# Optimization experiments

Measured on AMD Instinct MI355X. Metric: run time of the kernel, lower is better.

## Reference

```python
import jax, jax.numpy as jnp
import numpy as np

B, T, C, H, E, MIN_E = 4, 2048, 1024, 128, 16, 2
IS_CAUSAL = False


def setup_inputs() -> dict:
    key = jax.random.key(0)
    ks = jax.random.split(key, 6)
    lim_qkv = float(np.sqrt(6.0 / (C + H)))
    inp = {
        "hidden_states": jax.random.normal(ks[0], (B, T, C), jnp.float32),
        "sim_matrix": jax.random.normal(ks[1], (C, E), jnp.float32),
        "gates": jnp.zeros((E,), jnp.float32),
        "q_proj": jax.random.uniform(ks[2], (E, C, H), jnp.float32, -lim_qkv, lim_qkv),
        "k_proj": jax.random.uniform(ks[3], (E, C, H), jnp.float32, -lim_qkv, lim_qkv),
        "v_proj": jax.random.uniform(ks[4], (E, C, H), jnp.float32, -lim_qkv, lim_qkv),
        "o_proj": jax.random.uniform(ks[5], (E, H, C), jnp.float32, -lim_qkv, lim_qkv),
    }
    return inp


def _forward(hidden_states, sim_matrix, gates, q_proj, k_proj, v_proj, o_proj):
    b, t, c = hidden_states.shape
    n = b * t
    x = hidden_states.reshape(n, c)

    # ---- gating (faithful to _gating_logic) ----
    xn = x / jnp.maximum(jnp.linalg.norm(x, axis=-1, keepdims=True), 1e-12)
    sn = sim_matrix / jnp.maximum(jnp.linalg.norm(sim_matrix, axis=0, keepdims=True), 1e-12)
    logits = xn @ sn - jax.nn.sigmoid(gates)          # [n, E]
    gated = jax.nn.relu(logits)
    # STE: forward = (gated > 0), backward = identity
    hard = (gated > 0).astype(gated.dtype)
    mask = gated + jax.lax.stop_gradient(hard - gated)
    inactive = (jnp.sum(hard, axis=1) == 0)
    # fallback: top-MIN_E logits for tokens with no active expert
    _, fb_idx = jax.lax.top_k(logits, MIN_E)
    fb = jnp.zeros((n, logits.shape[1]), gated.dtype).at[
        jnp.arange(n)[:, None], fb_idx].set(1.0)
    put = jax.lax.stop_gradient(inactive[:, None].astype(gated.dtype) * fb)
    mask = mask * (1.0 - put) + put                   # index_put semantics
    masked = jnp.where(mask > 0, gated, -jnp.inf)
    w = jax.nn.softmax(masked, axis=-1)               # routing weights [n, E]

    # ---- MoE dispatch/combine (dense-equivalent: w is exactly 0 where mask==0) ----
    def moe_proj(p):  # p: [E, C, H] -> [n, H]
        y = jnp.einsum('nc,ech->neh', x, p)
        return jnp.einsum('ne,neh->nh', w, y)

    q = moe_proj(q_proj).reshape(b, t, -1)
    k = moe_proj(k_proj).reshape(b, t, -1)
    v = moe_proj(v_proj).reshape(b, t, -1)

    # single-head SDPA, default scale 1/sqrt(head_dim)
    h = q.shape[-1]
    scores = jnp.einsum('bth,bsh->bts', q, k) / jnp.sqrt(jnp.asarray(h, q.dtype))
    if IS_CAUSAL and t > 1:
        causal = jnp.tril(jnp.ones((t, t), bool))
        scores = jnp.where(causal[None], scores, -jnp.inf)
    attn = jax.nn.softmax(scores, axis=-1)
    o = jnp.einsum('bts,bsh->bth', attn, v).reshape(n, h)

    # output MoE combine
    z = jnp.einsum('ne,nh->enh', w, o)                # [E, n, H]
    out = jnp.einsum('enh,ehc->nc', z, o_proj)
    return out.reshape(b, t, c)


def reference(hidden_states, sim_matrix, gates, q_proj, k_proj, v_proj, o_proj):
    return _forward(hidden_states, sim_matrix, gates, q_proj, k_proj, v_proj, o_proj)
```

## Files before the change

### kernel.cpp

```cpp
#include <hip/hip_runtime.h>
#include <hip/hip_bf16.h>
#include <math.h>

#define NBATCH 4
#define NT     2048
#define NC     1024
#define NH     128
#define NE     16
#define NTOK   (NBATCH * NT)
#define CAP    18432
#define NT2_MAX 152

typedef __bf16 bf16x8 __attribute__((ext_vector_type(8)));
typedef __bf16 bf16x4 __attribute__((ext_vector_type(4)));
typedef float  f32x4  __attribute__((ext_vector_type(4)));

__device__ __forceinline__ __bf16 f2bf(float f) { return (__bf16)f; }

#define BARRIER() __builtin_amdgcn_s_barrier()
#define SFENCE()  __builtin_amdgcn_sched_barrier(0)
#define VMWAIT(n) asm volatile("s_waitcnt vmcnt(" #n ")" ::: "memory")
#define LGKMWAIT0() asm volatile("s_waitcnt lgkmcnt(0)" ::: "memory")

__device__ __forceinline__ void gl_lds16(const void* g, void* l) {
  __builtin_amdgcn_global_load_lds((const __attribute__((address_space(1))) void*)g,
                                   (__attribute__((address_space(3))) void*)l, 16, 0, 0);
}

__device__ __forceinline__ const __bf16* swz_src(const __bf16* row0, size_t stride,
                                                 int tid, int i) {
  int lin = (tid + 256 * i) * 16;
  int r = lin >> 7, cb = lin & 127;
  return row0 + (size_t)r * stride + ((cb ^ ((r & 7) << 4)) >> 1);
}

__global__ void k_transpose_all(const float* __restrict__ qp, const float* __restrict__ kp,
                                const float* __restrict__ vp, const float* __restrict__ op,
                                __bf16* __restrict__ pqt, __bf16* __restrict__ pkt,
                                __bf16* __restrict__ pvt, __bf16* __restrict__ pot,
                                const float* __restrict__ sim, const float* __restrict__ gates,
                                double* __restrict__ snorm, double* __restrict__ sig) {
  __shared__ float tile[32][33];
  __shared__ double red[16][17];
  int z = blockIdx.y;
  int tid = threadIdx.x;
  if (z == 64) {
    if (blockIdx.x != 0) return;
    int e = tid & 15, chunk = tid >> 4;
    double a = 0.0;
#pragma unroll 4
    for (int j = 0; j < 64; j++) {
      double v = (double)sim[(chunk * 64 + j) * NE + e];
      a += v * v;
    }
    red[chunk][e] = a;
    __syncthreads();
    if (tid < 16) {
      double s = 0.0;
      for (int k = 0; k < 16; k++) s += red[k][tid];
      snorm[tid] = fmax(sqrt(s), 1e-12);
      sig[tid] = 1.0 / (1.0 + exp(-(double)gates[tid]));
    }
    return;
  }
  const float* in;
  __bf16* out;
  int R, Cd, g, r0, c0;
  if (z < 48) {
    int which = z >> 4; g = z & 15; R = 1024; Cd = 128;
    in = which == 0 ? qp : (which == 1 ? kp : vp);
    out = which == 0 ? pqt : (which == 1 ? pkt : pvt);
    r0 = (blockIdx.x >> 2) * 32; c0 = (blockIdx.x & 3) * 32;
  } else {
    g = z - 48; R = 128; Cd = 1024;
    in = op; out = pot;
    r0 = (blockIdx.x & 3) * 32; c0 = (blockIdx.x >> 2) * 32;
  }
  int tx = tid & 31, ty0 = tid >> 5;
  const float* src = in + (size_t)g * R * Cd;
  __bf16* dst = out + (size_t)g * R * Cd;
#pragma unroll
  for (int ty = ty0; ty < 32; ty += 8)
    tile[ty][tx] = src[(size_t)(r0 + ty) * Cd + (c0 + tx)];
  __syncthreads();
#pragma unroll
  for (int ty = ty0; ty < 32; ty += 8)
    dst[(size_t)(c0 + ty) * R + (r0 + tx)] = f2bf(tile[tx][ty]);
}

__global__ __launch_bounds__(256, 2) void k_gating3(const float* __restrict__ x,
                                                    const float* __restrict__ sim,
                                                    const double* __restrict__ snorm,
                                                    const double* __restrict__ sig,
                                                    float* __restrict__ w_all,
                                                    int* __restrict__ counts,
                                                    __bf16* __restrict__ xbf) {
  __shared__ union {
    struct {
      float xs_[16][66];
      float ss_[16][66];
    } s;
    double red[8][32][2][17];
  } u;
  __shared__ float w_lds[16][16];
  __shared__ int cnt_lds[16];
  int tid = threadIdx.x;
  if (tid < 16) cnt_lds[tid] = 0;
  int cg = tid & 31, tkg = tid >> 5;
  int tok0 = blockIdx.x * 16;

  double acc[2][17];
#pragma unroll
  for (int t = 0; t < 2; t++)
#pragma unroll
    for (int i = 0; i < 17; i++) acc[t][i] = 0.0;

  int xr0 = tid >> 4, xc4 = (tid & 15) * 4;
  int sr = tid >> 2, se4 = (tid & 3) * 4;

  float4 xa, sv;
  auto ldchunk = [&](int c0) {
    xa = *(const float4*)(x + (size_t)(tok0 + xr0) * NC + c0 + xc4);
    sv = *(const float4*)(sim + (size_t)(c0 + sr) * NE + se4);
  };
  auto stchunk = [&]() {
    *(float4*)&u.s.xs_[xr0][xc4] = xa;
    u.s.ss_[se4 + 0][sr] = sv.x;
    u.s.ss_[se4 + 1][sr] = sv.y;
    u.s.ss_[se4 + 2][sr] = sv.z;
    u.s.ss_[se4 + 3][sr] = sv.w;
  };
  auto stxbf = [&](int c0) {
    bf16x4 a;
    a[0]=f2bf(xa.x); a[1]=f2bf(xa.y); a[2]=f2bf(xa.z); a[3]=f2bf(xa.w);
    *(bf16x4*)(xbf + (size_t)(tok0 + xr0) * NC + c0 + xc4) = a;
  };

  ldchunk(0);
  for (int ch = 0; ch < 16; ch++) {
    stchunk();
    stxbf(ch * 64);
    __syncthreads();
    if (ch < 15) ldchunk((ch + 1) * 64);
    double xd[2][2];
#pragma unroll
    for (int t = 0; t < 2; t++) {
      float2 xv = *(const float2*)&u.s.xs_[tkg * 2 + t][cg * 2];
      xd[t][0] = (double)xv.x;
      xd[t][1] = (double)xv.y;
      acc[t][16] += xd[t][0] * xd[t][0] + xd[t][1] * xd[t][1];
    }
#pragma unroll
    for (int e = 0; e < 16; e++) {
      float2 sv2 = *(const float2*)&u.s.ss_[e][cg * 2];
      double s0 = (double)sv2.x, s1 = (double)sv2.y;
#pragma unroll
      for (int t = 0; t < 2; t++)
        acc[t][e] += xd[t][0] * s0 + xd[t][1] * s1;
    }
    __syncthreads();
  }

#pragma unroll
  for (int t = 0; t < 2; t++)
#pragma unroll
    for (int i = 0; i < 17; i++)
      u.red[tkg][cg][t][i] = acc[t][i];
  __syncthreads();

  if (tid < 16) {
    double dots[17];
    for (int i = 0; i < 17; i++) {
      double s = 0.0;
      for (int c = 0; c < 32; c++) s += u.red[tid >> 1][c][tid & 1][i];
      dots[i] = s;
    }
    double xn = fmax(sqrt(dots[16]), 1e-12);
    double logits[NE];
    unsigned act = 0;
    int cnt = 0;
    for (int ee = 0; ee < NE; ee++) {
      logits[ee] = dots[ee] / (xn * snorm[ee]) - sig[ee];
      if (logits[ee] > 0.0) { act |= 1u << ee; cnt++; }
    }
    if (cnt == 0) {
      int i1 = 0; double b1 = logits[0];
      for (int ee = 1; ee < NE; ee++) if (logits[ee] > b1) { b1 = logits[ee]; i1 = ee; }
      int i2 = -1; double b2 = -1e300;
      for (int ee = 0; ee < NE; ee++) if (ee != i1 && logits[ee] > b2) { b2 = logits[ee]; i2 = ee; }
      act = (1u << i1) | (1u << i2);
    }
    double m = -1e300;
    for (int ee = 0; ee < NE; ee++) if ((act >> ee) & 1) m = fmax(m, fmax(logits[ee], 0.0));
    double s = 0.0, wvv[NE];
    for (int ee = 0; ee < NE; ee++) {
      if ((act >> ee) & 1) { wvv[ee] = exp(fmax(logits[ee], 0.0) - m); s += wvv[ee]; }
      else wvv[ee] = 0.0;
    }
    for (int ee = 0; ee < NE; ee++) {
      if ((act >> ee) & 1) {
        w_lds[tid][ee] = (float)(wvv[ee] / s);
        atomicAdd(&cnt_lds[ee], 1);
      } else w_lds[tid][ee] = 0.0f;
    }
  }
  __syncthreads();
  w_all[(size_t)(tok0 + (tid >> 4)) * NE + (tid & 15)] = w_lds[tid >> 4][tid & 15];
  if (tid < 16 && cnt_lds[tid] > 0) atomicAdd(&counts[tid], cnt_lds[tid]);
}

__global__ void k_transpose_bf(const __bf16* __restrict__ in, __bf16* __restrict__ out,
                               int R, int Cd) {
  __shared__ __bf16 tile[32][34];
  int g = blockIdx.z;
  int r0 = blockIdx.x * 32, c0 = blockIdx.y * 32;
  int tx = threadIdx.x & 31, ty0 = threadIdx.x >> 5;
  const __bf16* src = in + (size_t)g * R * Cd;
  __bf16* dst = out + (size_t)g * R * Cd;
#pragma unroll
  for (int ty = ty0; ty < 32; ty += 8)
    tile[ty][tx] = src[(size_t)(r0 + ty) * Cd + (c0 + tx)];
  __syncthreads();
#pragma unroll
  for (int ty = ty0; ty < 32; ty += 8)
    dst[(size_t)(c0 + ty) * R + (r0 + tx)] = tile[tx][ty];
}

__global__ void k_scan(const int* __restrict__ counts, int* __restrict__ offsets,
                       int2* __restrict__ tile_desc, int* __restrict__ n_tiles) {
  if (threadIdx.x == 0 && blockIdx.x == 0) {
    int off = 0, nt = 0;
    for (int e = 0; e < NE; e++) {
      offsets[e] = off;
      int c = counts[e];
      int tiles = (c + 127) >> 7;
      for (int t = 0; t < tiles; t++) {
        int s0 = off + t * 128;
        if (s0 < CAP && nt < NT2_MAX) { tile_desc[nt].x = e; tile_desc[nt].y = s0; nt++; }
      }
      off += c;
    }
    offsets[NE] = off;
    *n_tiles = nt;
  }
}

__global__ void k_assign(const float* __restrict__ w_all, const int* __restrict__ offsets,
                         int* __restrict__ cursors, int* __restrict__ slot_token,
                         float* __restrict__ slot_w, int* __restrict__ tok_slots,
                         int* __restrict__ tok_cnt) {
  int n = blockIdx.x * 256 + threadIdx.x;
  if (n >= NTOK) return;
  int j = 0;
  for (int e = 0; e < NE; e++) {
    float w = w_all[(size_t)n * NE + e];
    if (w > 0.0f) {
      int p = atomicAdd(&cursors[e], 1);
      int s = offsets[e] + p;
      slot_token[s] = n;
      slot_w[s] = w;
      tok_slots[n * 16 + j] = s;
      j++;
    }
  }
  tok_cnt[n] = j;
}

__device__ __forceinline__ void mfma_block(const __bf16* As, const __bf16* Bs,
                                           int lane, int wrow, f32x4 acc[8]) {
  const char* Ab = (const char*)As;
  const char* Bb = (const char*)Bs;
  int arow = wrow + (lane & 15);
  int rb = lane & 15;
#pragma unroll
  for (int ks = 0; ks < 2; ks++) {
    int kb = ks * 64 + (lane >> 4) * 16;
    bf16x8 af = *(const bf16x8*)(Ab + arow * 128 + (kb ^ ((arow & 7) << 4)));
#pragma unroll
    for (int nt = 0; nt < 8; nt++) {
      int brow = nt * 16 + rb;
      bf16x8 bv = *(const bf16x8*)(Bb + brow * 128 + (kb ^ ((brow & 7) << 4)));
      acc[nt] = __builtin_amdgcn_mfma_f32_16x16x32_bf16(af, bv, acc[nt], 0, 0, 0);
    }
  }
}

__device__ __forceinline__ void mfma_block128(const __bf16* As, const __bf16* Bs,
                                              int lane, int wrow2, f32x4 acc[2][8]) {
  const char* Ab = (const char*)As;
  const char* Bb = (const char*)Bs;
  int rb = lane & 15;
#pragma unroll
  for (int ks = 0; ks < 2; ks++) {
    int kb = ks * 64 + (lane >> 4) * 16;
    int ar = wrow2 + rb;
    int sw = kb ^ ((ar & 7) << 4);
    bf16x8 af0 = *(const bf16x8*)(Ab + ar * 128 + sw);
    bf16x8 af1 = *(const bf16x8*)(Ab + (ar + 16) * 128 + sw);
#pragma unroll
    for (int nt = 0; nt < 8; nt++) {
      int brow = nt * 16 + rb;
      bf16x8 bv = *(const bf16x8*)(Bb + brow * 128 + (kb ^ ((brow & 7) << 4)));
      acc[0][nt] = __builtin_amdgcn_mfma_f32_16x16x32_bf16(af0, bv, acc[0][nt], 0, 0, 0);
      acc[1][nt] = __builtin_amdgcn_mfma_f32_16x16x32_bf16(af1, bv, acc[1][nt], 0, 0, 0);
    }
  }
}

__device__ __forceinline__ void mfma_regA(bf16x8 af0, bf16x8 af1, const __bf16* Bs,
                                          int lane, f32x4 acc[8]) {
  const char* Bb = (const char*)Bs;
  int rb = lane & 15;
#pragma unroll
  for (int ks = 0; ks < 2; ks++) {
    int kb = ks * 64 + (lane >> 4) * 16;
    bf16x8 af = ks ? af1 : af0;
#pragma unroll
    for (int nt = 0; nt < 8; nt++) {
      int brow = nt * 16 + rb;
      bf16x8 bv = *(const bf16x8*)(Bb + brow * 128 + (kb ^ ((brow & 7) << 4)));
      acc[nt] = __builtin_amdgcn_mfma_f32_16x16x32_bf16(af, bv, acc[nt], 0, 0, 0);
    }
  }
}

__global__ __launch_bounds__(256) void k_moe_qkv2(
    const __bf16* __restrict__ xbf, const int* __restrict__ slot_token,
    const __bf16* __restrict__ pq, const __bf16* __restrict__ pk, const __bf16* __restrict__ pv,
    const int* __restrict__ offsets, const int2* __restrict__ tile_desc,
    const int* __restrict__ n_tiles,
    __bf16* __restrict__ yq, __bf16* __restrict__ yk, __bf16* __restrict__ yv) {
  int id = blockIdx.x;
  int w = (id & 7) * (3 * NT2_MAX / 8) + (id >> 3);
  int ti = w / 3, p = w % 3;
  if (ti >= *n_tiles) return;
  int2 td = tile_desc[ti];
  int e = td.x, s0 = td.y;
  int seg_end = offsets[e + 1]; if (seg_end > CAP) seg_end = CAP;
  const __bf16* Bt;
  __bf16* Yd;
  if (p == 0)      { Bt = pq; Yd = yq; }
  else if (p == 1) { Bt = pk; Yd = yk; }
  else             { Bt = pv; Yd = yv; }
  Bt += (size_t)e * NH * NC;

  __shared__ __bf16 As[2][128 * 64];
  __shared__ __bf16 Bs[2][128 * 64];
  int tid = threadIdx.x, lane = tid & 63, wid = tid >> 6, wrow2 = wid * 32;
  const __bf16* asrc[4];
  const __bf16* bsrc[4];
#pragma unroll
  for (int i = 0; i < 4; i++) {
    int lin = (tid + 256 * i) * 16;
    int r = lin >> 7, cb = lin & 127;
    int tok = slot_token[s0 + r] & (NTOK - 1);
    asrc[i] = xbf + (size_t)tok * NC + ((cb ^ ((r & 7) << 4)) >> 1);
  }
#pragma unroll
  for (int i = 0; i < 4; i++) bsrc[i] = swz_src(Bt, NC, tid, i);
  auto stage = [&](int buf, int k0) {
#pragma unroll
    for (int i = 0; i < 4; i++)
      gl_lds16(asrc[i] + k0, (char*)As[buf] + tid * 16 + i * 4096);
#pragma unroll
    for (int i = 0; i < 4; i++)
      gl_lds16(bsrc[i] + k0, (char*)Bs[buf] + tid * 16 + i * 4096);
  };

  f32x4 acc[2][8];
#pragma unroll
  for (int rf = 0; rf < 2; rf++)
#pragma unroll
    for (int i = 0; i < 8; i++) { f32x4 z = {0.f, 0.f, 0.f, 0.f}; acc[rf][i] = z; }

  stage(0, 0);
  stage(1, 64);
  VMWAIT(8); BARRIER(); SFENCE();
  int cur = 0;
  for (int t = 0; t <= 13; t++) {
    __builtin_amdgcn_s_setprio(1);
    mfma_block128(As[cur], Bs[cur], lane, wrow2, acc);
    __builtin_amdgcn_s_setprio(0);
    SFENCE();
    BARRIER();
    stage(cur, (t + 2) * 64);
    VMWAIT(8); BARRIER(); SFENCE();
    cur ^= 1;
  }
  __builtin_amdgcn_s_setprio(1);
  mfma_block128(As[cur], Bs[cur], lane, wrow2, acc);
  __builtin_amdgcn_s_setprio(0);
  SFENCE();
  VMWAIT(0); BARRIER(); SFENCE();
  __builtin_amdgcn_s_setprio(1);
  mfma_block128(As[cur ^ 1], Bs[cur ^ 1], lane, wrow2, acc);
  __builtin_amdgcn_s_setprio(0);

  int col = lane & 15, quad = lane >> 4;
#pragma unroll
  for (int rf = 0; rf < 2; rf++)
#pragma unroll
    for (int r = 0; r < 4; r++) {
      int s = s0 + wrow2 + rf * 16 + quad * 4 + r;
      if (s < seg_end) {
#pragma unroll
        for (int nt = 0; nt < 8; nt++)
          Yd[(size_t)s * NH + nt * 16 + col] = f2bf(acc[rf][nt][r]);
      }
    }
}

__global__ __launch_bounds__(256) void k_combine_qkv(
    const __bf16* __restrict__ yq, const __bf16* __restrict__ yk, const __bf16* __restrict__ yv,
    const int* __restrict__ tok_slots, const int* __restrict__ tok_cnt,
    const float* __restrict__ slot_w,
    __bf16* __restrict__ qb, __bf16* __restrict__ kb, __bf16* __restrict__ vb) {
  int token = blockIdx.x * 2 + (threadIdx.x >> 7);
  int h = threadIdx.x & 127;
  const __bf16* Y;
  __bf16* D;
  float sc = 1.0f;
  if (blockIdx.y == 0)      { Y = yq; D = qb; sc = 0.12751744458115337f; }
  else if (blockIdx.y == 1) { Y = yk; D = kb; }
  else                      { Y = yv; D = vb; }
  int cnt = tok_cnt[token];
  float acc = 0.f;
  for (int j = 0; j < cnt; j++) {
    int s = tok_slots[token * 16 + j];
    if (s < CAP) acc += slot_w[s] * (float)Y[(size_t)s * NH + h];
  }
  D[(size_t)token * NH + h] = f2bf(acc * sc);
}

__global__ __launch_bounds__(256) void k_flash(const __bf16* __restrict__ q,
                                               const __bf16* __restrict__ k,
                                               const __bf16* __restrict__ vt,
                                               float* __restrict__ opart,
                                               float2* __restrict__ ml) {
  int id = blockIdx.x;
  int w = (id & 7) * 64 + (id >> 3);
  int b = w >> 7;
  int rem = w & 127;
  int spl = rem >> 5;
  int t0 = (rem & 31) * 64;
  const __bf16* qb = q + (size_t)b * NT * NH;
  const __bf16* kb = k + (size_t)b * NT * NH;
  const __bf16* vtb = vt + (size_t)b * NH * NT;

  __shared__ __bf16 Ks[2][128 * 64];
  __shared__ __bf16 Vs[2][128 * 64];
  __shared__ __bf16 Ps[2][64 * 64];
  int tid = threadIdx.x, lane = tid & 63, wid = tid >> 6, wrow = wid * 16;
  int colq = lane & 15, quad = lane >> 4;

  bf16x8 qf[4];
  {
    const __bf16* qr = qb + (size_t)(t0 + wrow + colq) * NH + quad * 8;
#pragma unroll
    for (int kk = 0; kk < 4; kk++) qf[kk] = *(const bf16x8*)(qr + kk * 32);
  }
  asm volatile("" :: "v"(qf[0]), "v"(qf[1]), "v"(qf[2]), "v"(qf[3]));
  SFENCE();

  auto stage_K = [&](int s0) {
#pragma unroll
    for (int c = 0; c < 2; c++)
#pragma unroll
      for (int i = 0; i < 4; i++)
        gl_lds16(swz_src(kb + (size_t)s0 * NH + c * 64, NH, tid, i),
                 (char*)Ks[c] + wid * 1024 + i * 4096);
  };
  auto stage_V = [&](int s0) {
#pragma unroll
    for (int c = 0; c < 2; c++)
#pragma unroll
      for (int i = 0; i < 4; i++)
        gl_lds16(swz_src(vtb + s0 + c * 64, NT, tid, i),
                 (char*)Vs[c] + wid * 1024 + i * 4096);
  };

  f32x4 oacc[8];
#pragma unroll
  for (int i = 0; i < 8; i++) { f32x4 z = {0.f, 0.f, 0.f, 0.f}; oacc[i] = z; }
  float mr[4], lr[4];
#pragma unroll
  for (int r = 0; r < 4; r++) { mr[r] = -1e30f; lr[r] = 0.f; }

  const int sbase = spl * 512;
  stage_K(sbase);
  stage_V(sbase);
  VMWAIT(8); BARRIER(); SFENCE();

  for (int t = 0; t < 4; t++) {
    f32x4 sacc[8];
#pragma unroll
    for (int i = 0; i < 8; i++) { f32x4 z = {0.f, 0.f, 0.f, 0.f}; sacc[i] = z; }
    __builtin_amdgcn_s_setprio(1);
    mfma_regA(qf[0], qf[1], Ks[0], lane, sacc);
    mfma_regA(qf[2], qf[3], Ks[1], lane, sacc);
    __builtin_amdgcn_s_setprio(0);
    SFENCE();
    BARRIER();
    if (t < 3) stage_K(sbase + (t + 1) * 128);

    float tm[4];
#pragma unroll
    for (int r = 0; r < 4; r++) {
      float v = sacc[0][r];
#pragma unroll
      for (int nt = 1; nt < 8; nt++) v = fmaxf(v, sacc[nt][r]);
      tm[r] = v;
    }
#pragma unroll
    for (int off = 1; off < 16; off <<= 1)
#pragma unroll
      for (int r = 0; r < 4; r++) tm[r] = fmaxf(tm[r], __shfl_xor(tm[r], off));
    float alpha[4], rs[4];
#pragma unroll
    for (int r = 0; r < 4; r++) {
      float mn = fmaxf(mr[r], tm[r]);
      alpha[r] = exp2f(mr[r] - mn);
      mr[r] = mn;
      rs[r] = 0.f;
    }
#pragma unroll
    for (int nt = 0; nt < 8; nt++) {
      char* pc = (char*)Ps[nt >> 2];
      int colb = ((nt & 3) * 16 + colq) * 2;
#pragma unroll
      for (int r = 0; r < 4; r++) {
        int row = wrow + quad * 4 + r;
        float p = exp2f(sacc[nt][r] - mr[r]);
        rs[r] += p;
        *(__bf16*)(pc + row * 128 + (colb ^ ((row & 7) << 4))) = f2bf(p);
      }
    }
#pragma unroll
    for (int off = 1; off < 16; off <<= 1)
#pragma unroll
      for (int r = 0; r < 4; r++) rs[r] += __shfl_xor(rs[r], off);
#pragma unroll
    for (int r = 0; r < 4; r++) lr[r] = alpha[r] * lr[r] + rs[r];
#pragma unroll
    for (int nt = 0; nt < 8; nt++)
#pragma unroll
      for (int r = 0; r < 4; r++) oacc[nt][r] *= alpha[r];

    LGKMWAIT0();
    if (t < 3) { VMWAIT(8); } else { VMWAIT(0); }
    BARRIER(); SFENCE();

    __builtin_amdgcn_s_setprio(1);
    mfma_block(Ps[0], Vs[0], lane, wrow, oacc);
    mfma_block(Ps[1], Vs[1], lane, wrow, oacc);
    __builtin_amdgcn_s_setprio(0);
    SFENCE();
    BARRIER();
    if (t < 3) {
      stage_V(sbase + (t + 1) * 128);
      VMWAIT(8); BARRIER(); SFENCE();
    }
  }

  size_t base = (size_t)(b * 4 + spl) * NT + t0;
#pragma unroll
  for (int r = 0; r < 4; r++) {
    size_t row = base + wrow + quad * 4 + r;
#pragma unroll
    for (int nt = 0; nt < 8; nt++)
      opart[row * NH + nt * 16 + colq] = oacc[nt][r];
  }
  if (colq == 0) {
#pragma unroll
    for (int r = 0; r < 4; r++) {
      float2 v; v.x = mr[r]; v.y = lr[r];
      ml[base + wrow + quad * 4 + r] = v;
    }
  }
}

__global__ __launch_bounds__(256) void k_gather_o(const float* __restrict__ opart,
                                                  const float2* __restrict__ ml,
                                                  const int* __restrict__ slot_token,
                                                  const int* __restrict__ offsets,
                                                  __bf16* __restrict__ og) {
  int slot = blockIdx.x * 2 + (threadIdx.x >> 7);
  int h = threadIdx.x & 127;
  int total = offsets[NE]; if (total > CAP) total = CAP;
  if (slot >= total) return;
  int n = slot_token[slot];
  int b = n >> 11, trow = n & 2047;
  size_t rb = (size_t)b * 4 * NT + trow;
  float2 m0 = ml[rb], m1 = ml[rb + NT], m2 = ml[rb + 2 * NT], m3 = ml[rb + 3 * NT];
  float M = fmaxf(fmaxf(m0.x, m1.x), fmaxf(m2.x, m3.x));
  float e0 = exp2f(m0.x - M), e1 = exp2f(m1.x - M), e2 = exp2f(m2.x - M), e3 = exp2f(m3.x - M);
  float den = m0.y * e0 + m1.y * e1 + m2.y * e2 + m3.y * e3;
  float num = opart[rb * NH + h] * e0 + opart[(rb + NT) * NH + h] * e1 +
              opart[(rb + 2 * NT) * NH + h] * e2 + opart[(rb + 3 * NT) * NH + h] * e3;
  og[(size_t)slot * NH + h] = f2bf(num / den);
}

__global__ __launch_bounds__(256) void k_out2(
    const __bf16* __restrict__ og, const __bf16* __restrict__ pot,
    const int* __restrict__ offsets, const int2* __restrict__ tile_desc,
    const int* __restrict__ n_tiles, __bf16* __restrict__ zy) {
  int id = blockIdx.x;
  int w = (id & 7) * NT2_MAX + (id >> 3);
  int ti = w >> 3, p = w & 7;
  if (ti >= *n_tiles) return;
  int2 td = tile_desc[ti];
  int e = td.x, s0 = td.y;
  int seg_end = offsets[e + 1]; if (seg_end > CAP) seg_end = CAP;
  int nc0 = p * 128;
  const __bf16* Bt = pot + (size_t)e * NC * NH;

  __shared__ __bf16 As[2][128 * 64];
  __shared__ __bf16 Bs[2][128 * 64];
  int tid = threadIdx.x, lane = tid & 63, wid = tid >> 6, wrow2 = wid * 32;
  const __bf16* asrc[4];
  const __bf16* bsrc[4];
#pragma unroll
  for (int i = 0; i < 4; i++) asrc[i] = swz_src(og + (size_t)s0 * NH, NH, tid, i);
#pragma unroll
  for (int i = 0; i < 4; i++) bsrc[i] = swz_src(Bt + (size_t)nc0 * NH, NH, tid, i);
  auto stage = [&](int buf, int k0) {
#pragma unroll
    for (int i = 0; i < 4; i++)
      gl_lds16(asrc[i] + k0, (char*)As[buf] + tid * 16 + i * 4096);
#pragma unroll
    for (int i = 0; i < 4; i++)
      gl_lds16(bsrc[i] + k0, (char*)Bs[buf] + tid * 16 + i * 4096);
  };
  f32x4 acc[2][8];
#pragma unroll
  for (int rf = 0; rf < 2; rf++)
#pragma unroll
    for (int i = 0; i < 8; i++) { f32x4 z = {0.f, 0.f, 0.f, 0.f}; acc[rf][i] = z; }

  stage(0, 0);
  stage(1, 64);
  VMWAIT(8); BARRIER(); SFENCE();
  __builtin_amdgcn_s_setprio(1);
  mfma_block128(As[0], Bs[0], lane, wrow2, acc);
  __builtin_amdgcn_s_setprio(0);
  SFENCE();
  VMWAIT(0); BARRIER(); SFENCE();
  __builtin_amdgcn_s_setprio(1);
  mfma_block128(As[1], Bs[1], lane, wrow2, acc);
  __builtin_amdgcn_s_setprio(0);

  int col = lane & 15, quad = lane >> 4;
#pragma unroll
  for (int rf = 0; rf < 2; rf++)
#pragma unroll
    for (int r = 0; r < 4; r++) {
      int s = s0 + wrow2 + rf * 16 + quad * 4 + r;
      if (s < seg_end) {
#pragma unroll
        for (int nt = 0; nt < 8; nt++)
          zy[(size_t)s * NC + nc0 + nt * 16 + col] = f2bf(acc[rf][nt][r]);
      }
    }
}

__global__ __launch_bounds__(256) void k_combine_out(
    const __bf16* __restrict__ zy, const int* __restrict__ tok_slots,
    const int* __restrict__ tok_cnt, const float* __restrict__ slot_w,
    float* __restrict__ out) {
  int token = blockIdx.x;
  int c = threadIdx.x * 4;
  int cnt = tok_cnt[token];
  float a0 = 0.f, a1 = 0.f, a2 = 0.f, a3 = 0.f;
  for (int j = 0; j < cnt; j++) {
    int s = tok_slots[token * 16 + j];
    if (s < CAP) {
      float w = slot_w[s];
      bf16x4 z = *(const bf16x4*)&zy[(size_t)s * NC + c];
      a0 += w * (float)z[0];
      a1 += w * (float)z[1];
      a2 += w * (float)z[2];
      a3 += w * (float)z[3];
    }
  }
  float4 o = {a0, a1, a2, a3};
  *(float4*)&out[(size_t)token * NC + c] = o;
}

extern "C" void kernel_launch(void* const* d_in, const int* in_sizes, int n_in,
                              void* d_out, int out_size, void* d_ws, size_t ws_size,
                              hipStream_t stream) {
  const float* hs    = (const float*)d_in[0];
  const float* sim   = (const float*)d_in[1];
  const float* gates = (const float*)d_in[2];
  const float* qp    = (const float*)d_in[3];
  const float* kp    = (const float*)d_in[4];
  const float* vp    = (const float*)d_in[5];
  const float* op    = (const float*)d_in[6];
  float* out = (float*)d_out;
  char* ws = (char*)d_ws;

  const size_t M = 1048576;
  __bf16* PQT = (__bf16*)(ws + 0 * M);
  __bf16* PKT = (__bf16*)(ws + 4 * M);
  __bf16* PVT = (__bf16*)(ws + 8 * M);
  __bf16* POT = (__bf16*)(ws + 12 * M);
  __bf16* Qb  = (__bf16*)(ws + 16 * M);
  __bf16* Kb  = (__bf16*)(ws + 18 * M);
  __bf16* Vb  = (__bf16*)(ws + 20 * M);
  __bf16* VT  = (__bf16*)(ws + 22 * M);
  float*  WALL = (float*)(ws + 28 * M);
  int*    STOK = (int*)(ws + 28 * M + 524288);
  float*  SW   = (float*)(ws + 28 * M + 1048576);
  int*    TSL  = (int*)(ws + 28 * M + 1572864);
  int*    TCN  = (int*)(ws + 28 * M + 2097152);
  double* SNORM = (double*)(ws + 28 * M + 2129920);
  double* SIG   = SNORM + 16;
  int* CNT = (int*)(ws + 28 * M + 2130432);
  int* OFF = CNT + 16;
  int* CUR = CNT + 40;
  int* NTL = CNT + 60;
  int2* DESC = (int2*)(ws + 28 * M + 2131456);
  __bf16* XBF = (__bf16*)(ws + 32 * M);
  __bf16* YQ = (__bf16*)(ws + 72 * M);
  __bf16* YK = (__bf16*)(ws + 77 * M);
  __bf16* YV = (__bf16*)(ws + 82 * M);
  float*  OP2 = (float*)(ws + 32 * M);
  float2* MLB = (float2*)(ws + 50 * M);
  __bf16* OG = (__bf16*)(ws + 52 * M);
  __bf16* ZY = (__bf16*)(ws + 60 * M);

  hipMemsetAsync(CNT, 0, 512, stream);

  k_transpose_all<<<dim3(128, 65), 256, 0, stream>>>(qp, kp, vp, op, PQT, PKT, PVT, POT,
                                                     sim, gates, SNORM, SIG);
  k_gating3<<<NTOK / 16, 256, 0, stream>>>(hs, sim, SNORM, SIG, WALL, CNT, XBF);
  k_scan<<<1, 64, 0, stream>>>(CNT, OFF, DESC, NTL);
  k_assign<<<NTOK / 256, 256, 0, stream>>>(WALL, OFF, CUR, STOK, SW, TSL, TCN);
  k_moe_qkv2<<<3 * NT2_MAX, 256, 0, stream>>>(XBF, STOK, PQT, PKT, PVT, OFF, DESC, NTL, YQ, YK, YV);
  k_combine_qkv<<<dim3(NTOK / 2, 3), 256, 0, stream>>>(YQ, YK, YV, TSL, TCN, SW, Qb, Kb, Vb);
  k_transpose_bf<<<dim3(64, 4, 4), 256, 0, stream>>>(Vb, VT, 2048, 128);
  k_flash<<<512, 256, 0, stream>>>(Qb, Kb, VT, OP2, MLB);
  k_gather_o<<<CAP / 2, 256, 0, stream>>>(OP2, MLB, STOK, OFF, OG);
  k_out2<<<8 * NT2_MAX, 256, 0, stream>>>(OG, POT, OFF, DESC, NTL, ZY);
  k_combine_out<<<NTOK, 256, 0, stream>>>(ZY, TSL, TCN, SW, out);
}
```

Measured before the change: 286.2 us.

## Fuse V transpose into QKV combine, widen out-proj tiles, drop memset

The QKV combine kernel now handles 32 tokens per block with 16-wide vectorized bf16 loads. For V it transposes through LDS and writes V^T directly, which removes the separate transpose kernel and the Vb round trip. The output projection kernel computes two 128-column chunks per block, reusing the staged A tile and halving the grid. The counter memset is folded into the first kernel, saving one launch but adding ordering reliance on that kernel.

```diff
diff --git a/kernel.cpp b/kernel.cpp
--- a/kernel.cpp
+++ b/kernel.cpp
@@ -39,13 +39,15 @@
                                 __bf16* __restrict__ pqt, __bf16* __restrict__ pkt,
                                 __bf16* __restrict__ pvt, __bf16* __restrict__ pot,
                                 const float* __restrict__ sim, const float* __restrict__ gates,
-                                double* __restrict__ snorm, double* __restrict__ sig) {
+                                double* __restrict__ snorm, double* __restrict__ sig,
+                                int* __restrict__ ctrl) {
   __shared__ float tile[32][33];
   __shared__ double red[16][17];
   int z = blockIdx.y;
   int tid = threadIdx.x;
   if (z == 64) {
     if (blockIdx.x != 0) return;
+    if (tid < 128) ctrl[tid] = 0;
     int e = tid & 15, chunk = tid >> 4;
     double a = 0.0;
 #pragma unroll 4
@@ -209,23 +211,6 @@
   if (tid < 16 && cnt_lds[tid] > 0) atomicAdd(&counts[tid], cnt_lds[tid]);
 }
 
-__global__ void k_transpose_bf(const __bf16* __restrict__ in, __bf16* __restrict__ out,
-                               int R, int Cd) {
-  __shared__ __bf16 tile[32][34];
-  int g = blockIdx.z;
-  int r0 = blockIdx.x * 32, c0 = blockIdx.y * 32;
-  int tx = threadIdx.x & 31, ty0 = threadIdx.x >> 5;
-  const __bf16* src = in + (size_t)g * R * Cd;
-  __bf16* dst = out + (size_t)g * R * Cd;
-#pragma unroll
-  for (int ty = ty0; ty < 32; ty += 8)
-    tile[ty][tx] = src[(size_t)(r0 + ty) * Cd + (c0 + tx)];
-  __syncthreads();
-#pragma unroll
-  for (int ty = ty0; ty < 32; ty += 8)
-    dst[(size_t)(c0 + ty) * R + (r0 + tx)] = tile[tx][ty];
-}
-
 __global__ void k_scan(const int* __restrict__ counts, int* __restrict__ offsets,
                        int2* __restrict__ tile_desc, int* __restrict__ n_tiles) {
   if (threadIdx.x == 0 && blockIdx.x == 0) {
@@ -414,22 +399,49 @@
     const __bf16* __restrict__ yq, const __bf16* __restrict__ yk, const __bf16* __restrict__ yv,
     const int* __restrict__ tok_slots, const int* __restrict__ tok_cnt,
     const float* __restrict__ slot_w,
-    __bf16* __restrict__ qb, __bf16* __restrict__ kb, __bf16* __restrict__ vb) {
-  int token = blockIdx.x * 2 + (threadIdx.x >> 7);
-  int h = threadIdx.x & 127;
-  const __bf16* Y;
-  __bf16* D;
-  float sc = 1.0f;
-  if (blockIdx.y == 0)      { Y = yq; D = qb; sc = 0.12751744458115337f; }
-  else if (blockIdx.y == 1) { Y = yk; D = kb; }
-  else                      { Y = yv; D = vb; }
-  int cnt = tok_cnt[token];
-  float acc = 0.f;
+    __bf16* __restrict__ qb, __bf16* __restrict__ kb, __bf16* __restrict__ vt) {
+  __shared__ __bf16 vtile[128][34];
+  int tid = threadIdx.x;
+  int tok0 = blockIdx.x * 32;
+  int tt = tok0 + (tid >> 3);
+  int h0 = (tid & 7) * 16;
+  const __bf16* Y = blockIdx.y == 0 ? yq : (blockIdx.y == 1 ? yk : yv);
+  int cnt = tok_cnt[tt];
+  float acc[16];
+#pragma unroll
+  for (int i = 0; i < 16; i++) acc[i] = 0.f;
   for (int j = 0; j < cnt; j++) {
-    int s = tok_slots[token * 16 + j];
-    if (s < CAP) acc += slot_w[s] * (float)Y[(size_t)s * NH + h];
-  }
-  D[(size_t)token * NH + h] = f2bf(acc * sc);
+    int s = tok_slots[tt * 16 + j];
+    if (s < CAP) {
+      float w = slot_w[s];
+      bf16x8 v0 = *(const bf16x8*)(Y + (size_t)s * NH + h0);
+      bf16x8 v1 = *(const bf16x8*)(Y + (size_t)s * NH + h0 + 8);
+#pragma unroll
+      for (int i = 0; i < 8; i++) { acc[i] += w * (float)v0[i]; acc[8 + i] += w * (float)v1[i]; }
+    }
+  }
+  if (blockIdx.y == 2) {
+#pragma unroll
+    for (int i = 0; i < 16; i++) vtile[h0 + i][tid >> 3] = f2bf(acc[i]);
+    __syncthreads();
+    int h = tid >> 1, tp = (tid & 1) * 16;
+    int b = tok0 >> 11, trow = tok0 & 2047;
+    __bf16* dst = vt + ((size_t)b * NH + h) * NT + trow + tp;
+    bf16x8 o0, o1;
+#pragma unroll
+    for (int i = 0; i < 8; i++) { o0[i] = vtile[h][tp + i]; o1[i] = vtile[h][tp + 8 + i]; }
+    *(bf16x8*)dst = o0;
+    *(bf16x8*)(dst + 8) = o1;
+  } else {
+    float sc = blockIdx.y == 0 ? 0.12751744458115337f : 1.0f;
+    __bf16* D = blockIdx.y == 0 ? qb : kb;
+    bf16x8 o0, o1;
+#pragma unroll
+    for (int i = 0; i < 8; i++) { o0[i] = f2bf(acc[i] * sc); o1[i] = f2bf(acc[8 + i] * sc); }
+    __bf16* d = D + (size_t)tt * NH + h0;
+    *(bf16x8*)d = o0;
+    *(bf16x8*)(d + 8) = o1;
+  }
 }
 
 __global__ __launch_bounds__(256) void k_flash(const __bf16* __restrict__ q,
@@ -605,13 +617,13 @@
     const int* __restrict__ offsets, const int2* __restrict__ tile_desc,
     const int* __restrict__ n_tiles, __bf16* __restrict__ zy) {
   int id = blockIdx.x;
-  int w = (id & 7) * NT2_MAX + (id >> 3);
-  int ti = w >> 3, p = w & 7;
+  int w = (id & 7) * (4 * NT2_MAX / 8) + (id >> 3);
+  int ti = w >> 2, p = w & 3;
   if (ti >= *n_tiles) return;
   int2 td = tile_desc[ti];
   int e = td.x, s0 = td.y;
   int seg_end = offsets[e + 1]; if (seg_end > CAP) seg_end = CAP;
-  int nc0 = p * 128;
+  int nc0 = p * 256;
   const __bf16* Bt = pot + (size_t)e * NC * NH;
 
   __shared__ __bf16 As[2][128 * 64];
@@ -623,22 +635,39 @@
   for (int i = 0; i < 4; i++) asrc[i] = swz_src(og + (size_t)s0 * NH, NH, tid, i);
 #pragma unroll
   for (int i = 0; i < 4; i++) bsrc[i] = swz_src(Bt + (size_t)nc0 * NH, NH, tid, i);
-  auto stage = [&](int buf, int k0) {
+  auto stageA = [&](int buf, int k0) {
 #pragma unroll
     for (int i = 0; i < 4; i++)
       gl_lds16(asrc[i] + k0, (char*)As[buf] + tid * 16 + i * 4096);
+  };
+  auto stageB = [&](int buf, int k0, int noff) {
 #pragma unroll
     for (int i = 0; i < 4; i++)
-      gl_lds16(bsrc[i] + k0, (char*)Bs[buf] + tid * 16 + i * 4096);
+      gl_lds16(bsrc[i] + (size_t)noff * NH + k0, (char*)Bs[buf] + tid * 16 + i * 4096);
   };
   f32x4 acc[2][8];
+  int col = lane & 15, quad = lane >> 4;
+  auto store_acc = [&](int nco) {
+#pragma unroll
+    for (int rf = 0; rf < 2; rf++)
+#pragma unroll
+      for (int r = 0; r < 4; r++) {
+        int s = s0 + wrow2 + rf * 16 + quad * 4 + r;
+        if (s < seg_end) {
+#pragma unroll
+          for (int nt = 0; nt < 8; nt++)
+            zy[(size_t)s * NC + nco + nt * 16 + col] = f2bf(acc[rf][nt][r]);
+        }
+      }
+  };
+
 #pragma unroll
   for (int rf = 0; rf < 2; rf++)
 #pragma unroll
     for (int i = 0; i < 8; i++) { f32x4 z = {0.f, 0.f, 0.f, 0.f}; acc[rf][i] = z; }
 
-  stage(0, 0);
-  stage(1, 64);
+  stageA(0, 0); stageB(0, 0, 0);
+  stageA(1, 64); stageB(1, 64, 0);
   VMWAIT(8); BARRIER(); SFENCE();
   __builtin_amdgcn_s_setprio(1);
   mfma_block128(As[0], Bs[0], lane, wrow2, acc);
@@ -648,19 +677,20 @@
   __builtin_amdgcn_s_setprio(1);
   mfma_block128(As[1], Bs[1], lane, wrow2, acc);
   __builtin_amdgcn_s_setprio(0);
-
-  int col = lane & 15, quad = lane >> 4;
+  SFENCE();
+  store_acc(nc0);
+  BARRIER();
+  stageB(0, 0, 128); stageB(1, 64, 128);
 #pragma unroll
   for (int rf = 0; rf < 2; rf++)
 #pragma unroll
-    for (int r = 0; r < 4; r++) {
-      int s = s0 + wrow2 + rf * 16 + quad * 4 + r;
-      if (s < seg_end) {
-#pragma unroll
-        for (int nt = 0; nt < 8; nt++)
-          zy[(size_t)s * NC + nc0 + nt * 16 + col] = f2bf(acc[rf][nt][r]);
-      }
-    }
+    for (int i = 0; i < 8; i++) { f32x4 z = {0.f, 0.f, 0.f, 0.f}; acc[rf][i] = z; }
+  VMWAIT(0); BARRIER(); SFENCE();
+  __builtin_amdgcn_s_setprio(1);
+  mfma_block128(As[0], Bs[0], lane, wrow2, acc);
+  mfma_block128(As[1], Bs[1], lane, wrow2, acc);
+  __builtin_amdgcn_s_setprio(0);
+  store_acc(nc0 + 128);
 }
 
 __global__ __launch_bounds__(256) void k_combine_out(
@@ -706,7 +736,6 @@
   __bf16* POT = (__bf16*)(ws + 12 * M);
   __bf16* Qb  = (__bf16*)(ws + 16 * M);
   __bf16* Kb  = (__bf16*)(ws + 18 * M);
-  __bf16* Vb  = (__bf16*)(ws + 20 * M);
   __bf16* VT  = (__bf16*)(ws + 22 * M);
   float*  WALL = (float*)(ws + 28 * M);
   int*    STOK = (int*)(ws + 28 * M + 524288);
@@ -729,18 +758,15 @@
   __bf16* OG = (__bf16*)(ws + 52 * M);
   __bf16* ZY = (__bf16*)(ws + 60 * M);
 
-  hipMemsetAsync(CNT, 0, 512, stream);
-
   k_transpose_all<<<dim3(128, 65), 256, 0, stream>>>(qp, kp, vp, op, PQT, PKT, PVT, POT,
-                                                     sim, gates, SNORM, SIG);
+                                                     sim, gates, SNORM, SIG, CNT);
   k_gating3<<<NTOK / 16, 256, 0, stream>>>(hs, sim, SNORM, SIG, WALL, CNT, XBF);
   k_scan<<<1, 64, 0, stream>>>(CNT, OFF, DESC, NTL);
   k_assign<<<NTOK / 256, 256, 0, stream>>>(WALL, OFF, CUR, STOK, SW, TSL, TCN);
   k_moe_qkv2<<<3 * NT2_MAX, 256, 0, stream>>>(XBF, STOK, PQT, PKT, PVT, OFF, DESC, NTL, YQ, YK, YV);
-  k_combine_qkv<<<dim3(NTOK / 2, 3), 256, 0, stream>>>(YQ, YK, YV, TSL, TCN, SW, Qb, Kb, Vb);
-  k_transpose_bf<<<dim3(64, 4, 4), 256, 0, stream>>>(Vb, VT, 2048, 128);
+  k_combine_qkv<<<dim3(NTOK / 32, 3), 256, 0, stream>>>(YQ, YK, YV, TSL, TCN, SW, Qb, Kb, VT);
   k_flash<<<512, 256, 0, stream>>>(Qb, Kb, VT, OP2, MLB);
   k_gather_o<<<CAP / 2, 256, 0, stream>>>(OP2, MLB, STOK, OFF, OG);
-  k_out2<<<8 * NT2_MAX, 256, 0, stream>>>(OG, POT, OFF, DESC, NTL, ZY);
+  k_out2<<<4 * NT2_MAX, 256, 0, stream>>>(OG, POT, OFF, DESC, NTL, ZY);
   k_combine_out<<<NTOK, 256, 0, stream>>>(ZY, TSL, TCN, SW, out);
 }
```

After: 273.5 us. 1.05x faster.
